# Kernel optimization log

Measured on AMD Instinct MI355X. Metric: run time of the kernel, lower is better.

The kernel has to match this reference:

```python
import jax, jax.numpy as jnp
import numpy as np

N_NODES = 50000


def spmm(rows, cols, vals, dense):
    # out[i,:] = sum_{e: rows[e]==i} vals[e] * dense[cols[e], :]
    gathered = dense[cols] * vals[:, None]  # [E, D]
    return jax.ops.segment_sum(gathered, rows, num_segments=N_NODES)


def setup_inputs() -> dict:
    key = jax.random.key(0)
    k1, k2, k3, k4, k5, k6 = jax.random.split(key, 6)
    N, E, F, H, C = N_NODES, 800000, 512, 256, 64
    node_features = jax.random.normal(k1, (N, F), dtype=jnp.float32)
    adj_rows = jax.random.randint(k2, (E,), 0, N, dtype=jnp.int32)
    adj_cols = jax.random.randint(k3, (E,), 0, N, dtype=jnp.int32)
    adj_vals = jax.random.uniform(k4, (E,), dtype=jnp.float32)
    W1 = jax.random.normal(k5, (F, H), dtype=jnp.float32) * (1.0 / np.sqrt(F))
    b1 = jnp.zeros((H,), dtype=jnp.float32)
    W2 = jax.random.normal(k6, (H, C), dtype=jnp.float32) * (1.0 / np.sqrt(H))
    b2 = jnp.zeros((C,), dtype=jnp.float32)
    return {"node_features": node_features, "adj_rows": adj_rows,
            "adj_cols": adj_cols, "adj_vals": adj_vals,
            "W1": W1, "b1": b1, "W2": W2, "b2": b2}


def reference(node_features, adj_rows, adj_cols, adj_vals, W1, b1, W2, b2):
    # Layer 1: dense projection then sparse aggregation, then ReLU.
    support1 = node_features @ W1 + b1           # [N, H]
    x = jax.nn.relu(spmm(adj_rows, adj_cols, adj_vals, support1))
    # Dropout is identity in eval mode (training=False).
    # Layer 2
    support2 = x @ W2 + b2                       # [N, C]
    x = spmm(adj_rows, adj_cols, adj_vals, support2)
    return jax.nn.log_softmax(x, axis=1)
```

## Files before the change

kernel.cpp:

```cpp
#include <hip/hip_runtime.h>

#define N_NODES 50000
#define N_EDGES 800000
#define F_IN    512
#define H_DIM   256
#define C_DIM   64
#define MPAD    50048

#define NB      196
#define NCHUNK  49
#define CHUNK   16384
#define BCAP    6144

typedef __bf16 bf16;
typedef __bf16 bf16x4 __attribute__((ext_vector_type(4)));
typedef __bf16 bf16x8 __attribute__((ext_vector_type(8)));
typedef float  f32x4  __attribute__((ext_vector_type(4)));
typedef unsigned int u32;
typedef unsigned char u8;

__device__ __forceinline__ void gl_lds16(const void* g, void* l) {
    __builtin_amdgcn_global_load_lds(
        (const __attribute__((address_space(1))) u32*)g,
        (__attribute__((address_space(3))) u32*)l, 16, 0, 0);
}

__device__ __forceinline__ float unpack_val(u32 pk) {
    return __builtin_bit_cast(float, pk << 16);
}


__global__ __launch_bounds__(1024) void histA_k(const int* __restrict__ rows,
                                                u32* __restrict__ G) {
    __shared__ u32 h[16 * NB];
    int tid = threadIdx.x, wid = tid >> 6;
    for (int i = tid; i < 16 * NB; i += 1024) h[i] = 0;
    __syncthreads();
    int base = blockIdx.x * CHUNK;
    int end = base + CHUNK; if (end > N_EDGES) end = N_EDGES;
    for (int e = base + tid; e < end; e += 1024)
        atomicAdd(&h[wid * NB + (rows[e] >> 8)], 1);
    __syncthreads();
    if (tid < NB) {
        u32 s = 0;
#pragma unroll
        for (int w = 0; w < 16; w++) s += h[w * NB + tid];
        G[tid * NCHUNK + blockIdx.x] = s;
    }
}

__global__ __launch_bounds__(1024) void scatterB_k(const int* __restrict__ rows,
                                                   const int* __restrict__ cols,
                                                   const float* __restrict__ vals,
                                                   const u32* __restrict__ G,
                                                   u32* __restrict__ epack,
                                                   u8* __restrict__ lrow) {
    __shared__ u32 cur[NB];
    __shared__ u32 wtot[16];
    int tid = threadIdx.x, wid = tid >> 6, lane = tid & 63;
    int c = blockIdx.x;
    u32 tot = 0, pre = 0;
    if (tid < NB) {
        for (int cc = 0; cc < NCHUNK; cc++) {
            u32 v = G[tid * NCHUNK + cc];
            tot += v;
            if (cc < c) pre += v;
        }
    }
    u32 incl = tot;
#pragma unroll
    for (int off = 1; off < 64; off <<= 1) {
        u32 u = __shfl_up(incl, off, 64);
        if (lane >= off) incl += u;
    }
    if (lane == 63) wtot[wid] = incl;
    __syncthreads();
    u32 wpre = 0;
#pragma unroll
    for (int w = 0; w < 16; w++)
        if (w < wid) wpre += wtot[w];
    if (tid < NB) cur[tid] = (wpre + incl - tot) + pre;
    __syncthreads();
    int base = c * CHUNK;
    int end = base + CHUNK; if (end > N_EDGES) end = N_EDGES;
    for (int e = base + tid; e < end; e += 1024) {
        int r = rows[e];
        unsigned short vb = __builtin_bit_cast(unsigned short, (bf16)vals[e]);
        u32 pk = ((u32)cols[e] << 16) | (u32)vb;
        u32 p = atomicAdd(&cur[r >> 8], 1);
        epack[p] = pk;
        lrow[p] = (u8)(r & 255);
    }
}

__global__ __launch_bounds__(256) void sortC_k(u32* __restrict__ epack,
                                               const u8* __restrict__ lrow,
                                               const u32* __restrict__ G,
                                               int* __restrict__ starts) {
    __shared__ u32 edat[BCAP];
    __shared__ u32 sdat[BCAP];
    __shared__ u8  erow[BCAP];
    __shared__ u32 h[4 * 256];
    __shared__ u32 cur[256];
    __shared__ u32 wt1[4], wt2[4];
    __shared__ u32 sh_s, sh_n;
    int b = blockIdx.x, tid = threadIdx.x, wid = tid >> 6, lane = tid & 63;

    u32 btot = 0;
    if (tid < NB)
        for (int cc = 0; cc < NCHUNK; cc++) btot += G[tid * NCHUNK + cc];
    u32 bincl = btot;
#pragma unroll
    for (int off = 1; off < 64; off <<= 1) {
        u32 u = __shfl_up(bincl, off, 64);
        if (lane >= off) bincl += u;
    }
    if (lane == 63) wt1[wid] = bincl;
    __syncthreads();
    u32 bwpre = 0;
#pragma unroll
    for (int w = 0; w < 4; w++)
        if (w < wid) bwpre += wt1[w];
    if (tid == b) { sh_s = bwpre + bincl - btot; sh_n = btot; }
    __syncthreads();
    int s = (int)sh_s;
    int n = (int)sh_n;
    if (n > BCAP) n = BCAP;

    for (int i = tid; i < n; i += 256) { edat[i] = epack[s + i]; erow[i] = lrow[s + i]; }
    for (int i = tid; i < 1024; i += 256) h[i] = 0;
    __syncthreads();
    for (int i = tid; i < n; i += 256) atomicAdd(&h[wid * 256 + erow[i]], 1);
    __syncthreads();
    u32 tot = h[tid] + h[256 + tid] + h[512 + tid] + h[768 + tid];
    u32 incl = tot;
#pragma unroll
    for (int off = 1; off < 64; off <<= 1) {
        u32 u = __shfl_up(incl, off, 64);
        if (lane >= off) incl += u;
    }
    if (lane == 63) wt2[wid] = incl;
    __syncthreads();
    u32 wpre = 0;
#pragma unroll
    for (int w = 0; w < 4; w++)
        if (w < wid) wpre += wt2[w];
    u32 excl = wpre + incl - tot;
    cur[tid] = excl;
    int grow = b * 256 + tid;
    if (grow < N_NODES) starts[grow] = s + (int)excl;
    if (b == 0 && tid == 0) starts[N_NODES] = N_EDGES;
    __syncthreads();
    for (int i = tid; i < n; i += 256) {
        u32 p = atomicAdd(&cur[erow[i]], 1);
        sdat[p] = edat[i];
    }
    __syncthreads();
    for (int i = tid; i < n; i += 256) epack[s + i] = sdat[i];
}


__global__ __launch_bounds__(256) void tr_w_k(const float* __restrict__ W1,
                                              const float* __restrict__ W2,
                                              bf16* __restrict__ W1t,
                                              bf16* __restrict__ W2t) {
    int i = blockIdx.x * 256 + threadIdx.x;
    if (i < F_IN * H_DIM) {
        int k = i >> 8, n = i & 255;
        W1t[n * F_IN + k] = (bf16)W1[i];
    } else {
        int j = i - F_IN * H_DIM;
        int k = j >> 6, n = j & 63;
        W2t[n * H_DIM + k] = (bf16)W2[j];
    }
}


__global__ __launch_bounds__(512) void gemm1_k(const float* __restrict__ A,
                                               const bf16* __restrict__ Bt,
                                               const float* __restrict__ bias,
                                               bf16* __restrict__ C) {
    constexpr int BM = 128, BN = 256, BK = 64;
    __shared__ bf16 As[BM * BK];
    __shared__ bf16 Bs[BN * BK];

    int tid = threadIdx.x;
    int wid = tid >> 6, lane = tid & 63;
    int wr = wid >> 2, wc = wid & 3;
    int bm = blockIdx.x;

    f32x4 acc[4][4];
#pragma unroll
    for (int m = 0; m < 4; m++)
#pragma unroll
        for (int n = 0; n < 4; n++) acc[m][n] = (f32x4){0.f, 0.f, 0.f, 0.f};

    for (int kt = 0; kt < F_IN; kt += BK) {
#pragma unroll
        for (int j = 0; j < 4; j++) {
            int ch = j * 512 + tid;
            int row = ch >> 3, kc = ch & 7;
            gl_lds16(Bt + (size_t)row * F_IN + kt + kc * 8,
                     &Bs[(j * 512 + wid * 64) * 8]);
        }
#pragma unroll
        for (int j = 0; j < 2; j++) {
            int ch = j * 512 + tid;
            int row = ch >> 3, kc = ch & 7;
            int ar = bm * BM + row;
            if (ar >= N_NODES) ar = N_NODES - 1;
            const f32x4* src = (const f32x4*)(A + (size_t)ar * F_IN + kt + kc * 8);
            f32x4 u = src[0], v = src[1];
            bf16x8 o;
            o[0] = (bf16)u[0]; o[1] = (bf16)u[1]; o[2] = (bf16)u[2]; o[3] = (bf16)u[3];
            o[4] = (bf16)v[0]; o[5] = (bf16)v[1]; o[6] = (bf16)v[2]; o[7] = (bf16)v[3];
            *(bf16x8*)&As[(size_t)ch * 8] = o;
        }
        __syncthreads();

        bf16x8 afr[2][4], bfr[2][4];
#pragma unroll
        for (int kk = 0; kk < 2; kk++) {
#pragma unroll
            for (int m = 0; m < 4; m++)
                afr[kk][m] = *(const bf16x8*)&As[(wr * 64 + m * 16 + (lane & 15)) * BK +
                                                 kk * 32 + (lane >> 4) * 8];
#pragma unroll
            for (int n = 0; n < 4; n++)
                bfr[kk][n] = *(const bf16x8*)&Bs[(wc * 64 + n * 16 + (lane & 15)) * BK +
                                                 kk * 32 + (lane >> 4) * 8];
        }
#pragma unroll
        for (int kk = 0; kk < 2; kk++)
#pragma unroll
            for (int m = 0; m < 4; m++)
#pragma unroll
                for (int n = 0; n < 4; n++)
                    acc[m][n] = __builtin_amdgcn_mfma_f32_16x16x32_bf16(
                        afr[kk][m], bfr[kk][n], acc[m][n], 0, 0, 0);
        __syncthreads();
    }

#pragma unroll
    for (int m = 0; m < 4; m++) {
        int row0 = bm * BM + wr * 64 + m * 16 + (lane >> 4) * 4;
#pragma unroll
        for (int n = 0; n < 4; n++) {
            int col = wc * 64 + n * 16 + (lane & 15);
            float bz = bias[col];
#pragma unroll
            for (int r = 0; r < 4; r++) {
                int row = row0 + r;
                if (row < N_NODES)
                    C[(size_t)row * H_DIM + col] = (bf16)(acc[m][n][r] + bz);
            }
        }
    }
}


__global__ __launch_bounds__(256) void gemm2_k(const bf16* __restrict__ A,
                                               const bf16* __restrict__ Bt,
                                               const float* __restrict__ bias,
                                               bf16* __restrict__ C) {
    constexpr int BM = 128, BK = 64;
    __shared__ bf16 As[BM * BK];
    __shared__ bf16 Bs[64 * BK];

    int tid = threadIdx.x;
    int wid = tid >> 6, lane = tid & 63;
    int wr = wid >> 1, wc = wid & 1;
    int bm = blockIdx.x;

    f32x4 acc[4][2];
#pragma unroll
    for (int m = 0; m < 4; m++)
#pragma unroll
        for (int n = 0; n < 2; n++) acc[m][n] = (f32x4){0.f, 0.f, 0.f, 0.f};

    for (int kt = 0; kt < H_DIM; kt += BK) {
#pragma unroll
        for (int j = 0; j < 4; j++) {
            int ch = j * 256 + tid;
            int row = ch >> 3, kc = ch & 7;
            gl_lds16(A + (size_t)(bm * BM + row) * H_DIM + kt + kc * 8,
                     &As[(j * 256 + wid * 64) * 8]);
        }
#pragma unroll
        for (int j = 0; j < 2; j++) {
            int ch = j * 256 + tid;
            int row = ch >> 3, kc = ch & 7;
            gl_lds16(Bt + (size_t)row * H_DIM + kt + kc * 8,
                     &Bs[(j * 256 + wid * 64) * 8]);
        }
        __syncthreads();

        bf16x8 afr[2][4], bfr[2][2];
#pragma unroll
        for (int kk = 0; kk < 2; kk++) {
#pragma unroll
            for (int m = 0; m < 4; m++)
                afr[kk][m] = *(const bf16x8*)&As[(wr * 64 + m * 16 + (lane & 15)) * BK +
                                                 kk * 32 + (lane >> 4) * 8];
#pragma unroll
            for (int n = 0; n < 2; n++)
                bfr[kk][n] = *(const bf16x8*)&Bs[(wc * 32 + n * 16 + (lane & 15)) * BK +
                                                 kk * 32 + (lane >> 4) * 8];
        }
#pragma unroll
        for (int kk = 0; kk < 2; kk++)
#pragma unroll
            for (int m = 0; m < 4; m++)
#pragma unroll
                for (int n = 0; n < 2; n++)
                    acc[m][n] = __builtin_amdgcn_mfma_f32_16x16x32_bf16(
                        afr[kk][m], bfr[kk][n], acc[m][n], 0, 0, 0);
        __syncthreads();
    }

#pragma unroll
    for (int m = 0; m < 4; m++) {
        int row0 = bm * BM + wr * 64 + m * 16 + (lane >> 4) * 4;
#pragma unroll
        for (int n = 0; n < 2; n++) {
            int col = wc * 32 + n * 16 + (lane & 15);
            float bz = bias[col];
#pragma unroll
            for (int r = 0; r < 4; r++) {
                int row = row0 + r;
                if (row < N_NODES)
                    C[(size_t)row * C_DIM + col] = (bf16)(acc[m][n][r] + bz);
            }
        }
    }
}


__global__ __launch_bounds__(256) void spmm1_k(const int* __restrict__ starts,
                                               const u32* __restrict__ epack,
                                               const bf16* __restrict__ s1,
                                               bf16* __restrict__ x16) {
    int wid = threadIdx.x >> 6, lane = threadIdx.x & 63;
    int row = blockIdx.x * 4 + wid;
    if (row >= N_NODES) return;
    int s = starts[row], e = starts[row + 1];
    f32x4 acc = (f32x4){0.f, 0.f, 0.f, 0.f};
    const bf16* s1l = s1 + lane * 4;
    int p = s;
    for (; p + 8 <= e; p += 8) {
        u32 k0 = epack[p],     k1 = epack[p + 1], k2 = epack[p + 2], k3 = epack[p + 3];
        u32 k4 = epack[p + 4], k5 = epack[p + 5], k6 = epack[p + 6], k7 = epack[p + 7];
        bf16x4 g0 = *(const bf16x4*)(s1l + (size_t)(k0 >> 16) * H_DIM);
        bf16x4 g1 = *(const bf16x4*)(s1l + (size_t)(k1 >> 16) * H_DIM);
        bf16x4 g2 = *(const bf16x4*)(s1l + (size_t)(k2 >> 16) * H_DIM);
        bf16x4 g3 = *(const bf16x4*)(s1l + (size_t)(k3 >> 16) * H_DIM);
        bf16x4 g4 = *(const bf16x4*)(s1l + (size_t)(k4 >> 16) * H_DIM);
        bf16x4 g5 = *(const bf16x4*)(s1l + (size_t)(k5 >> 16) * H_DIM);
        bf16x4 g6 = *(const bf16x4*)(s1l + (size_t)(k6 >> 16) * H_DIM);
        bf16x4 g7 = *(const bf16x4*)(s1l + (size_t)(k7 >> 16) * H_DIM);
        float v0 = unpack_val(k0), v1 = unpack_val(k1), v2 = unpack_val(k2), v3 = unpack_val(k3);
        float v4 = unpack_val(k4), v5 = unpack_val(k5), v6 = unpack_val(k6), v7 = unpack_val(k7);
#pragma unroll
        for (int j = 0; j < 4; j++)
            acc[j] += v0 * (float)g0[j] + v1 * (float)g1[j] +
                      v2 * (float)g2[j] + v3 * (float)g3[j] +
                      v4 * (float)g4[j] + v5 * (float)g5[j] +
                      v6 * (float)g6[j] + v7 * (float)g7[j];
    }
    for (; p < e; ++p) {
        u32 k = epack[p];
        float v = unpack_val(k);
        bf16x4 g = *(const bf16x4*)(s1l + (size_t)(k >> 16) * H_DIM);
#pragma unroll
        for (int j = 0; j < 4; j++) acc[j] += v * (float)g[j];
    }
    bf16x4 o;
#pragma unroll
    for (int j = 0; j < 4; j++) o[j] = (bf16)fmaxf(acc[j], 0.f);
    *(bf16x4*)(x16 + (size_t)row * H_DIM + lane * 4) = o;
}


__global__ __launch_bounds__(256) void spmm2_sm_k(const int* __restrict__ starts,
                                                  const u32* __restrict__ epack,
                                                  const bf16* __restrict__ s2,
                                                  float* __restrict__ out) {
    int wid = threadIdx.x >> 6, lane = threadIdx.x & 63;
    int row = blockIdx.x * 4 + wid;
    if (row >= N_NODES) return;
    int s = starts[row], e = starts[row + 1];
    float acc = 0.f;
    int p = s;
    for (; p + 8 <= e; p += 8) {
        u32 k0 = epack[p],     k1 = epack[p + 1], k2 = epack[p + 2], k3 = epack[p + 3];
        u32 k4 = epack[p + 4], k5 = epack[p + 5], k6 = epack[p + 6], k7 = epack[p + 7];
        float g0 = (float)s2[(size_t)(k0 >> 16) * C_DIM + lane];
        float g1 = (float)s2[(size_t)(k1 >> 16) * C_DIM + lane];
        float g2 = (float)s2[(size_t)(k2 >> 16) * C_DIM + lane];
        float g3 = (float)s2[(size_t)(k3 >> 16) * C_DIM + lane];
        float g4 = (float)s2[(size_t)(k4 >> 16) * C_DIM + lane];
        float g5 = (float)s2[(size_t)(k5 >> 16) * C_DIM + lane];
        float g6 = (float)s2[(size_t)(k6 >> 16) * C_DIM + lane];
        float g7 = (float)s2[(size_t)(k7 >> 16) * C_DIM + lane];
        acc += unpack_val(k0) * g0 + unpack_val(k1) * g1 +
               unpack_val(k2) * g2 + unpack_val(k3) * g3 +
               unpack_val(k4) * g4 + unpack_val(k5) * g5 +
               unpack_val(k6) * g6 + unpack_val(k7) * g7;
    }
    for (; p < e; ++p) {
        u32 k = epack[p];
        acc += unpack_val(k) * (float)s2[(size_t)(k >> 16) * C_DIM + lane];
    }
    float mx = acc;
#pragma unroll
    for (int off = 32; off >= 1; off >>= 1) mx = fmaxf(mx, __shfl_xor(mx, off, 64));
    float ex = expf(acc - mx);
    float se = ex;
#pragma unroll
    for (int off = 32; off >= 1; off >>= 1) se += __shfl_xor(se, off, 64);
    out[(size_t)row * C_DIM + lane] = (acc - mx) - logf(se);
}


extern "C" void kernel_launch(void* const* d_in, const int* in_sizes, int n_in,
                              void* d_out, int out_size, void* d_ws, size_t ws_size,
                              hipStream_t stream) {
    const float* nf   = (const float*)d_in[0];
    const int*   rows = (const int*)d_in[1];
    const int*   cols = (const int*)d_in[2];
    const float* vals = (const float*)d_in[3];
    const float* W1   = (const float*)d_in[4];
    const float* b1   = (const float*)d_in[5];
    const float* W2   = (const float*)d_in[6];
    const float* b2   = (const float*)d_in[7];
    float* out = (float*)d_out;

    char* w = (char*)d_ws;
    auto alloc = [&](size_t b) { void* p = (void*)w; w += (b + 255) & ~(size_t)255; return p; };

    bf16* x16  = (bf16*)alloc((size_t)MPAD * H_DIM * 2);
    bf16* sup1 = (bf16*)alloc((size_t)N_NODES * H_DIM * 2);
    bf16* sup2 = sup1;
    bf16* W1t = (bf16*)alloc((size_t)H_DIM * F_IN * 2);
    bf16* W2t = (bf16*)alloc((size_t)C_DIM * H_DIM * 2);
    int* starts = (int*)alloc((size_t)(N_NODES + 1) * 4);
    u32* G      = (u32*)alloc((size_t)NB * NCHUNK * 4);
    u32* epack  = (u32*)alloc((size_t)N_EDGES * 4);
    u8*  lrow   = (u8*)alloc((size_t)N_EDGES);

    histA_k<<<NCHUNK, 1024, 0, stream>>>(rows, G);
    scatterB_k<<<NCHUNK, 1024, 0, stream>>>(rows, cols, vals, G, epack, lrow);
    sortC_k<<<NB, 256, 0, stream>>>(epack, lrow, G, starts);

    tr_w_k<<<(F_IN * H_DIM + H_DIM * C_DIM) / 256, 256, 0, stream>>>(W1, W2, W1t, W2t);

    gemm1_k<<<MPAD / 128, 512, 0, stream>>>(nf, W1t, b1, sup1);
    spmm1_k<<<(N_NODES + 3) / 4, 256, 0, stream>>>(starts, epack, sup1, x16);

    gemm2_k<<<MPAD / 128, 256, 0, stream>>>(x16, W2t, b2, sup2);
    spmm2_sm_k<<<(N_NODES + 3) / 4, 256, 0, stream>>>(starts, epack, sup2, out);

    (void)in_sizes; (void)n_in; (void)out_size; (void)ws_size;
}
```

Before: 190.7 us.

## Fuse histogram with weight transpose and bucket sort with GEMM1 into shared launches

```diff
diff --git a/kernel.cpp b/kernel.cpp
--- a/kernel.cpp
+++ b/kernel.cpp
@@ -17,6 +17,7 @@
 typedef __bf16 bf16x8 __attribute__((ext_vector_type(8)));
 typedef float  f32x4  __attribute__((ext_vector_type(4)));
 typedef unsigned int u32;
+typedef unsigned long long u64;
 typedef unsigned char u8;
 
 __device__ __forceinline__ void gl_lds16(const void* g, void* l) {
@@ -30,24 +31,44 @@
 }
 
 
-__global__ __launch_bounds__(1024) void histA_k(const int* __restrict__ rows,
-                                                u32* __restrict__ G) {
+__global__ __launch_bounds__(1024) void prep_k(const int* __restrict__ rows,
+                                               const float* __restrict__ W1,
+                                               const float* __restrict__ W2,
+                                               u32* __restrict__ G,
+                                               bf16* __restrict__ W1t,
+                                               bf16* __restrict__ W2t) {
     __shared__ u32 h[16 * NB];
-    int tid = threadIdx.x, wid = tid >> 6;
-    for (int i = tid; i < 16 * NB; i += 1024) h[i] = 0;
-    __syncthreads();
-    int base = blockIdx.x * CHUNK;
-    int end = base + CHUNK; if (end > N_EDGES) end = N_EDGES;
-    for (int e = base + tid; e < end; e += 1024)
-        atomicAdd(&h[wid * NB + (rows[e] >> 8)], 1);
-    __syncthreads();
-    if (tid < NB) {
-        u32 s = 0;
-#pragma unroll
-        for (int w = 0; w < 16; w++) s += h[w * NB + tid];
-        G[tid * NCHUNK + blockIdx.x] = s;
-    }
-}
+    int bid = blockIdx.x, tid = threadIdx.x;
+    if (bid < NCHUNK) {
+        int wid = tid >> 6;
+        for (int i = tid; i < 16 * NB; i += 1024) h[i] = 0;
+        __syncthreads();
+        int base = bid * CHUNK;
+        int end = base + CHUNK; if (end > N_EDGES) end = N_EDGES;
+        for (int e = base + tid; e < end; e += 1024)
+            atomicAdd(&h[wid * NB + (rows[e] >> 8)], 1);
+        __syncthreads();
+        if (tid < NB) {
+            u32 s = 0;
+#pragma unroll
+            for (int w = 0; w < 16; w++) s += h[w * NB + tid];
+            G[tid * NCHUNK + bid] = s;
+        }
+    } else {
+        int i = (bid - NCHUNK) * 1024 + tid;
+        if (i < F_IN * H_DIM) {
+            int k = i >> 8, n = i & 255;
+            W1t[n * F_IN + k] = (bf16)W1[i];
+        } else {
+            int j = i - F_IN * H_DIM;
+            if (j < H_DIM * C_DIM) {
+                int k = j >> 6, n = j & 63;
+                W2t[n * H_DIM + k] = (bf16)W2[j];
+            }
+        }
+    }
+}
+
 
 __global__ __launch_bounds__(1024) void scatterB_k(const int* __restrict__ rows,
                                                    const int* __restrict__ cols,
@@ -93,101 +114,98 @@
     }
 }
 
-__global__ __launch_bounds__(256) void sortC_k(u32* __restrict__ epack,
-                                               const u8* __restrict__ lrow,
-                                               const u32* __restrict__ G,
-                                               int* __restrict__ starts) {
-    __shared__ u32 edat[BCAP];
-    __shared__ u32 sdat[BCAP];
-    __shared__ u8  erow[BCAP];
-    __shared__ u32 h[4 * 256];
-    __shared__ u32 cur[256];
-    __shared__ u32 wt1[4], wt2[4];
-    __shared__ u32 sh_s, sh_n;
-    int b = blockIdx.x, tid = threadIdx.x, wid = tid >> 6, lane = tid & 63;
-
-    u32 btot = 0;
-    if (tid < NB)
-        for (int cc = 0; cc < NCHUNK; cc++) btot += G[tid * NCHUNK + cc];
-    u32 bincl = btot;
-#pragma unroll
-    for (int off = 1; off < 64; off <<= 1) {
-        u32 u = __shfl_up(bincl, off, 64);
-        if (lane >= off) bincl += u;
-    }
-    if (lane == 63) wt1[wid] = bincl;
-    __syncthreads();
-    u32 bwpre = 0;
-#pragma unroll
-    for (int w = 0; w < 4; w++)
-        if (w < wid) bwpre += wt1[w];
-    if (tid == b) { sh_s = bwpre + bincl - btot; sh_n = btot; }
-    __syncthreads();
-    int s = (int)sh_s;
-    int n = (int)sh_n;
-    if (n > BCAP) n = BCAP;
-
-    for (int i = tid; i < n; i += 256) { edat[i] = epack[s + i]; erow[i] = lrow[s + i]; }
-    for (int i = tid; i < 1024; i += 256) h[i] = 0;
-    __syncthreads();
-    for (int i = tid; i < n; i += 256) atomicAdd(&h[wid * 256 + erow[i]], 1);
-    __syncthreads();
-    u32 tot = h[tid] + h[256 + tid] + h[512 + tid] + h[768 + tid];
-    u32 incl = tot;
-#pragma unroll
-    for (int off = 1; off < 64; off <<= 1) {
-        u32 u = __shfl_up(incl, off, 64);
-        if (lane >= off) incl += u;
-    }
-    if (lane == 63) wt2[wid] = incl;
-    __syncthreads();
-    u32 wpre = 0;
-#pragma unroll
-    for (int w = 0; w < 4; w++)
-        if (w < wid) wpre += wt2[w];
-    u32 excl = wpre + incl - tot;
-    cur[tid] = excl;
-    int grow = b * 256 + tid;
-    if (grow < N_NODES) starts[grow] = s + (int)excl;
-    if (b == 0 && tid == 0) starts[N_NODES] = N_EDGES;
-    __syncthreads();
-    for (int i = tid; i < n; i += 256) {
-        u32 p = atomicAdd(&cur[erow[i]], 1);
-        sdat[p] = edat[i];
-    }
-    __syncthreads();
-    for (int i = tid; i < n; i += 256) epack[s + i] = sdat[i];
-}
-
-
-__global__ __launch_bounds__(256) void tr_w_k(const float* __restrict__ W1,
-                                              const float* __restrict__ W2,
-                                              bf16* __restrict__ W1t,
-                                              bf16* __restrict__ W2t) {
-    int i = blockIdx.x * 256 + threadIdx.x;
-    if (i < F_IN * H_DIM) {
-        int k = i >> 8, n = i & 255;
-        W1t[n * F_IN + k] = (bf16)W1[i];
-    } else {
-        int j = i - F_IN * H_DIM;
-        int k = j >> 6, n = j & 63;
-        W2t[n * H_DIM + k] = (bf16)W2[j];
-    }
-}
-
-
-__global__ __launch_bounds__(512) void gemm1_k(const float* __restrict__ A,
-                                               const bf16* __restrict__ Bt,
-                                               const float* __restrict__ bias,
-                                               bf16* __restrict__ C) {
-    constexpr int BM = 128, BN = 256, BK = 64;
-    __shared__ bf16 As[BM * BK];
-    __shared__ bf16 Bs[BN * BK];
-
-    int tid = threadIdx.x;
-    int wid = tid >> 6, lane = tid & 63;
+
+__global__ __launch_bounds__(512) void sg1_k(u32* __restrict__ epack,
+                                             const u8* __restrict__ lrow,
+                                             const u32* __restrict__ G,
+                                             int* __restrict__ starts,
+                                             const float* __restrict__ A,
+                                             const bf16* __restrict__ Bt,
+                                             const float* __restrict__ bias,
+                                             bf16* __restrict__ C) {
+    __shared__ __attribute__((aligned(16))) char smem[49152];
+    int bid = blockIdx.x, tid = threadIdx.x, wid = tid >> 6, lane = tid & 63;
+
+    if (bid < NB) {
+        u32* sdat = (u32*)smem;
+        u8*  erow = (u8*)(smem + 24576);
+        u32* h    = (u32*)(smem + 30720);
+        u32* cur  = (u32*)(smem + 38912);
+        u32* wt1  = (u32*)(smem + 39936);
+        u32* wt2  = (u32*)(smem + 39968);
+        u32* shsn = (u32*)(smem + 40000);
+        int b = bid;
+
+        if (tid < 256) {
+            u32 btot = 0;
+            if (tid < NB)
+                for (int cc = 0; cc < NCHUNK; cc++) btot += G[tid * NCHUNK + cc];
+            u32 bincl = btot;
+#pragma unroll
+            for (int off = 1; off < 64; off <<= 1) {
+                u32 u = __shfl_up(bincl, off, 64);
+                if (lane >= off) bincl += u;
+            }
+            if (lane == 63) wt1[wid] = bincl;
+            __syncthreads();
+            u32 bwpre = 0;
+#pragma unroll
+            for (int w = 0; w < 4; w++)
+                if (w < wid) bwpre += wt1[w];
+            if (tid == b) { shsn[0] = bwpre + bincl - btot; shsn[1] = btot; }
+        } else {
+            __syncthreads();
+        }
+        __syncthreads();
+        int s = (int)shsn[0];
+        int n = (int)shsn[1];
+        if (n > BCAP) n = BCAP;
+
+        for (int i = tid; i < n; i += 512) erow[i] = lrow[s + i];
+        for (int i = tid; i < 2048; i += 512) h[i] = 0;
+        __syncthreads();
+        for (int i = tid; i < n; i += 512) atomicAdd(&h[wid * 256 + erow[i]], 1);
+        __syncthreads();
+        if (tid < 256) {
+            u32 tot = 0;
+#pragma unroll
+            for (int w = 0; w < 8; w++) tot += h[w * 256 + tid];
+            u32 incl = tot;
+#pragma unroll
+            for (int off = 1; off < 64; off <<= 1) {
+                u32 u = __shfl_up(incl, off, 64);
+                if (lane >= off) incl += u;
+            }
+            if (lane == 63) wt2[wid] = incl;
+            __syncthreads();
+            u32 wpre = 0;
+#pragma unroll
+            for (int w = 0; w < 4; w++)
+                if (w < wid) wpre += wt2[w];
+            u32 excl = wpre + incl - tot;
+            cur[tid] = excl;
+            int grow = b * 256 + tid;
+            if (grow < N_NODES) starts[grow] = s + (int)excl;
+        } else {
+            __syncthreads();
+        }
+        if (b == 0 && tid == 0) starts[N_NODES] = N_EDGES;
+        __syncthreads();
+        for (int i = tid; i < n; i += 512) {
+            u32 v = epack[s + i];
+            u32 p = atomicAdd(&cur[erow[i]], 1);
+            sdat[p] = v;
+        }
+        __syncthreads();
+        for (int i = tid; i < n; i += 512) epack[s + i] = sdat[i];
+        return;
+    }
+
+    bf16* As = (bf16*)smem;
+    bf16* Bs = (bf16*)(smem + 16384);
+    constexpr int BM = 128, BK = 64;
     int wr = wid >> 2, wc = wid & 3;
-    int bm = blockIdx.x;
+    int bm = bid - NB;
 
     f32x4 acc[4][4];
 #pragma unroll
@@ -348,8 +366,14 @@
     const bf16* s1l = s1 + lane * 4;
     int p = s;
     for (; p + 8 <= e; p += 8) {
-        u32 k0 = epack[p],     k1 = epack[p + 1], k2 = epack[p + 2], k3 = epack[p + 3];
-        u32 k4 = epack[p + 4], k5 = epack[p + 5], k6 = epack[p + 6], k7 = epack[p + 7];
+        u32 k0 = __builtin_nontemporal_load(epack + p);
+        u32 k1 = __builtin_nontemporal_load(epack + p + 1);
+        u32 k2 = __builtin_nontemporal_load(epack + p + 2);
+        u32 k3 = __builtin_nontemporal_load(epack + p + 3);
+        u32 k4 = __builtin_nontemporal_load(epack + p + 4);
+        u32 k5 = __builtin_nontemporal_load(epack + p + 5);
+        u32 k6 = __builtin_nontemporal_load(epack + p + 6);
+        u32 k7 = __builtin_nontemporal_load(epack + p + 7);
         bf16x4 g0 = *(const bf16x4*)(s1l + (size_t)(k0 >> 16) * H_DIM);
         bf16x4 g1 = *(const bf16x4*)(s1l + (size_t)(k1 >> 16) * H_DIM);
         bf16x4 g2 = *(const bf16x4*)(s1l + (size_t)(k2 >> 16) * H_DIM);
@@ -368,7 +392,7 @@
                       v6 * (float)g6[j] + v7 * (float)g7[j];
     }
     for (; p < e; ++p) {
-        u32 k = epack[p];
+        u32 k = __builtin_nontemporal_load(epack + p);
         float v = unpack_val(k);
         bf16x4 g = *(const bf16x4*)(s1l + (size_t)(k >> 16) * H_DIM);
 #pragma unroll
@@ -377,7 +401,8 @@
     bf16x4 o;
 #pragma unroll
     for (int j = 0; j < 4; j++) o[j] = (bf16)fmaxf(acc[j], 0.f);
-    *(bf16x4*)(x16 + (size_t)row * H_DIM + lane * 4) = o;
+    u64 bits = __builtin_bit_cast(u64, o);
+    __builtin_nontemporal_store(bits, (u64*)(x16 + (size_t)row * H_DIM + lane * 4));
 }
 
 
@@ -392,8 +417,14 @@
     float acc = 0.f;
     int p = s;
     for (; p + 8 <= e; p += 8) {
-        u32 k0 = epack[p],     k1 = epack[p + 1], k2 = epack[p + 2], k3 = epack[p + 3];
-        u32 k4 = epack[p + 4], k5 = epack[p + 5], k6 = epack[p + 6], k7 = epack[p + 7];
+        u32 k0 = __builtin_nontemporal_load(epack + p);
+        u32 k1 = __builtin_nontemporal_load(epack + p + 1);
+        u32 k2 = __builtin_nontemporal_load(epack + p + 2);
+        u32 k3 = __builtin_nontemporal_load(epack + p + 3);
+        u32 k4 = __builtin_nontemporal_load(epack + p + 4);
+        u32 k5 = __builtin_nontemporal_load(epack + p + 5);
+        u32 k6 = __builtin_nontemporal_load(epack + p + 6);
+        u32 k7 = __builtin_nontemporal_load(epack + p + 7);
         float g0 = (float)s2[(size_t)(k0 >> 16) * C_DIM + lane];
         float g1 = (float)s2[(size_t)(k1 >> 16) * C_DIM + lane];
         float g2 = (float)s2[(size_t)(k2 >> 16) * C_DIM + lane];
@@ -408,7 +439,7 @@
                unpack_val(k6) * g6 + unpack_val(k7) * g7;
     }
     for (; p < e; ++p) {
-        u32 k = epack[p];
+        u32 k = __builtin_nontemporal_load(epack + p);
         acc += unpack_val(k) * (float)s2[(size_t)(k >> 16) * C_DIM + lane];
     }
     float mx = acc;
@@ -418,7 +449,8 @@
     float se = ex;
 #pragma unroll
     for (int off = 32; off >= 1; off >>= 1) se += __shfl_xor(se, off, 64);
-    out[(size_t)row * C_DIM + lane] = (acc - mx) - logf(se);
+    __builtin_nontemporal_store((acc - mx) - logf(se),
+                                out + (size_t)row * C_DIM + lane);
 }
 
 
@@ -448,15 +480,10 @@
     u32* epack  = (u32*)alloc((size_t)N_EDGES * 4);
     u8*  lrow   = (u8*)alloc((size_t)N_EDGES);
 
-    histA_k<<<NCHUNK, 1024, 0, stream>>>(rows, G);
+    prep_k<<<NCHUNK + 144, 1024, 0, stream>>>(rows, W1, W2, G, W1t, W2t);
     scatterB_k<<<NCHUNK, 1024, 0, stream>>>(rows, cols, vals, G, epack, lrow);
-    sortC_k<<<NB, 256, 0, stream>>>(epack, lrow, G, starts);
-
-    tr_w_k<<<(F_IN * H_DIM + H_DIM * C_DIM) / 256, 256, 0, stream>>>(W1, W2, W1t, W2t);
-
-    gemm1_k<<<MPAD / 128, 512, 0, stream>>>(nf, W1t, b1, sup1);
+    sg1_k<<<NB + MPAD / 128, 512, 0, stream>>>(epack, lrow, G, starts, nf, W1t, b1, sup1);
     spmm1_k<<<(N_NODES + 3) / 4, 256, 0, stream>>>(starts, epack, sup1, x16);
-
     gemm2_k<<<MPAD / 128, 256, 0, stream>>>(x16, W2t, b2, sup2);
     spmm2_sm_k<<<(N_NODES + 3) / 4, 256, 0, stream>>>(starts, epack, sup2, out);
 
```

After: 194.8 us. 1.02x slower.
